# Kernel optimization log

Measured on AMD Instinct MI355X. Metric: run time of the kernel, lower is better.

## Reference

```python
import jax, jax.numpy as jnp
import numpy as np

N = 2048          # nodes == tokens
D_IN = 768        # input_size
H = 768           # hidden_size
OUT = 128         # output_size
NUM_LEVELS = int(np.floor(np.log2(N))) + 1  # heap tree height + 1 = 12


def _build_tree():
    # binary-heap tree: parent of node i (i>0) is (i-1)//2; node 0 is root
    parent = np.array([(i - 1) // 2 for i in range(1, N)], dtype=np.int64)
    child = np.arange(1, N, dtype=np.int64)
    # node_order = subtree height (leaves = 0), computed bottom-up
    node_order = np.zeros(N, dtype=np.int64)
    for i in range(N - 1, 0, -1):
        p = (i - 1) // 2
        node_order[p] = max(node_order[p], node_order[i] + 1)
    adjacency_list = np.stack([parent, child], axis=1)  # [E,2] (parent, child)
    edge_order = node_order[parent]                     # level of the parent
    return node_order, adjacency_list, edge_order


def setup_inputs() -> dict:
    key = jax.random.key(0)
    ks = jax.random.split(key, 16)
    s_in = 1.0 / np.sqrt(D_IN)
    s_h = 1.0 / np.sqrt(H)
    node_order, adjacency_list, edge_order = _build_tree()
    return {
        "tree_features": jax.random.normal(ks[0], (N, D_IN), jnp.float32),
        "features_tensor": jax.random.normal(ks[1], (N, D_IN), jnp.float32),
        # TreeLSTM params (child-sum)
        "W_iou": jax.random.normal(ks[2], (3 * H, D_IN), jnp.float32) * s_in,
        "b_iou": jax.random.normal(ks[3], (3 * H,), jnp.float32) * s_in,
        "U_iou": jax.random.normal(ks[4], (3 * H, H), jnp.float32) * s_h,
        "W_f": jax.random.normal(ks[5], (H, D_IN), jnp.float32) * s_in,
        "b_f": jax.random.normal(ks[6], (H,), jnp.float32) * s_in,
        "U_f": jax.random.normal(ks[7], (H, H), jnp.float32) * s_h,
        # nn.LSTM params (single layer, gate order i,f,g,o)
        "W_ih": jax.random.normal(ks[8], (4 * H, D_IN), jnp.float32) * s_h,
        "b_ih": jax.random.normal(ks[9], (4 * H,), jnp.float32) * s_h,
        "W_hh": jax.random.normal(ks[10], (4 * H, H), jnp.float32) * s_h,
        "b_hh": jax.random.normal(ks[11], (4 * H,), jnp.float32) * s_h,
        # classifier
        "W_cls": jax.random.normal(ks[12], (OUT, 2 * H), jnp.float32) * (1.0 / np.sqrt(2 * H)),
        "b_cls": jax.random.normal(ks[13], (OUT,), jnp.float32) * (1.0 / np.sqrt(2 * H)),
        "node_order": jnp.asarray(node_order),
        "adjacency_list": jnp.asarray(adjacency_list),
        "edge_order": jnp.asarray(edge_order),
    }


def _tree_lstm(x, node_order, adjacency_list, edge_order, W_iou, b_iou, U_iou, W_f, b_f, U_f):
    n, h_dim = x.shape[0], U_f.shape[0]
    x_iou = x @ W_iou.T + b_iou   # [N,3H]
    x_f = x @ W_f.T + b_f         # [N,H]
    parent = adjacency_list[:, 0]
    child = adjacency_list[:, 1]
    h = jnp.zeros((n, h_dim), x.dtype)
    c = jnp.zeros((n, h_dim), x.dtype)
    for lvl in range(NUM_LEVELS):
        emask = (edge_order == lvl).astype(x.dtype)[:, None]   # [E,1]
        child_h = h[child]
        child_c = c[child]
        h_sum = jax.ops.segment_sum(child_h * emask, parent, num_segments=n)
        iou = x_iou + h_sum @ U_iou.T
        i, o, u = jnp.split(iou, 3, axis=1)
        i = jax.nn.sigmoid(i); o = jax.nn.sigmoid(o); u = jnp.tanh(u)
        f = jax.nn.sigmoid(x_f[parent] + child_h @ U_f.T)       # per-edge forget gate
        c_sum = jax.ops.segment_sum(f * child_c * emask, parent, num_segments=n)
        c_new = i * u + c_sum
        h_new = o * jnp.tanh(c_new)
        nmask = (node_order == lvl)[:, None]
        h = jnp.where(nmask, h_new, h)
        c = jnp.where(nmask, c_new, c)
    return h, c


def _seq_lstm(x, W_ih, b_ih, W_hh, b_hh):
    h_dim = W_hh.shape[1]
    def step(carry, x_t):
        h_t, c_t = carry
        g = W_ih @ x_t + b_ih + W_hh @ h_t + b_hh
        i, f, gg, o = jnp.split(g, 4)
        i = jax.nn.sigmoid(i); f = jax.nn.sigmoid(f)
        gg = jnp.tanh(gg); o = jax.nn.sigmoid(o)
        c_t = f * c_t + i * gg
        h_t = o * jnp.tanh(c_t)
        return (h_t, c_t), h_t
    init = (jnp.zeros((h_dim,), x.dtype), jnp.zeros((h_dim,), x.dtype))
    _, hs = jax.lax.scan(step, init, x)
    return hs  # [N,H]


def reference(tree_features, features_tensor, W_iou, b_iou, U_iou, W_f, b_f, U_f,
              W_ih, b_ih, W_hh, b_hh, W_cls, b_cls,
              node_order, adjacency_list, edge_order):
    tree_h, _ = _tree_lstm(tree_features, node_order, adjacency_list, edge_order,
                           W_iou, b_iou, U_iou, W_f, b_f, U_f)
    lstm_h = _seq_lstm(features_tensor, W_ih, b_ih, W_hh, b_hh)
    cls_in = jnp.concatenate([tree_h, lstm_h], axis=1)          # [N,2H]
    logits = cls_in @ W_cls.T + b_cls                           # [N,OUT]
    return jax.nn.log_softmax(logits, axis=0)                   # LogSoftmax over dim=0
```

## Files before the change

### kernel.cpp

```cpp
#include <hip/hip_runtime.h>
#include <stdint.h>


typedef __bf16 bf16x8 __attribute__((ext_vector_type(8)));
typedef float  f32x4  __attribute__((ext_vector_type(4)));
typedef unsigned long long u64;

__device__ __forceinline__ float bf2f(uint16_t v) {
    return __uint_as_float(((uint32_t)v) << 16);
}
__device__ __forceinline__ uint16_t f2bf(float f) {
    uint32_t u = __float_as_uint(f);
    uint32_t r = (u + 0x7fffu + ((u >> 16) & 1u)) >> 16;
    return (uint16_t)r;
}
__device__ __forceinline__ float sigf(float x) { return 1.0f / (1.0f + __expf(-x)); }
__device__ __forceinline__ float tanh_f(float x) {
    x = fminf(fmaxf(x, -15.0f), 15.0f);
    float e = __expf(2.0f * x);
    return (e - 1.0f) / (e + 1.0f);
}

__global__ __launch_bounds__(256)
void detect_mode(const uint16_t* __restrict__ p, int* __restrict__ mode)
{
    int i = blockIdx.x * 256 + threadIdx.x;
    uint16_t v = p[i];
    bool bad = ((v >> 7) & 0xFF) == 0xFF;
    if (__ballot(bad) != 0ull) {
        if ((threadIdx.x & 63) == 0) atomicOr(mode, 1);
    }
}

struct ConvArgs {
    const void* src[14];
    void*       dst[14];
    int         n[14];
};

__global__ __launch_bounds__(256)
void conv_canon(ConvArgs a, const int* __restrict__ mode)
{
    int t = blockIdx.y;
    int n = a.n[t];
    int i = (blockIdx.x * 256 + threadIdx.x) * 8;
    if (i >= n) return;
    uint16_t* d = (uint16_t*)a.dst[t] + i;
    if (*mode) {
        const float* s = (const float*)a.src[t] + i;
        float4 v0 = reinterpret_cast<const float4*>(s)[0];
        float4 v1 = reinterpret_cast<const float4*>(s)[1];
        d[0] = f2bf(v0.x); d[1] = f2bf(v0.y); d[2] = f2bf(v0.z); d[3] = f2bf(v0.w);
        d[4] = f2bf(v1.x); d[5] = f2bf(v1.y); d[6] = f2bf(v1.z); d[7] = f2bf(v1.w);
    } else {
        *reinterpret_cast<uint4*>(d) =
            *reinterpret_cast<const uint4*>((const uint16_t*)a.src[t] + i);
    }
}

__global__ __launch_bounds__(256)
void gemm_pre(const uint16_t* __restrict__ treeF, const uint16_t* __restrict__ featF,
              const uint16_t* __restrict__ W_iou, const uint16_t* __restrict__ b_iou,
              const uint16_t* __restrict__ W_f,   const uint16_t* __restrict__ b_f,
              const uint16_t* __restrict__ W_ih,  const uint16_t* __restrict__ b_ih,
              const uint16_t* __restrict__ b_hh,
              uint16_t* __restrict__ x_iou, uint16_t* __restrict__ x_f,
              uint16_t* __restrict__ seq_pre)
{
    int lane = threadIdx.x & 63;
    int wave = threadIdx.x >> 6;
    int colTile = blockIdx.x * 4 + wave;
    int row0 = blockIdx.y * 16;
    int cl = lane & 15, quad = lane >> 4;
    int colg = colTile * 16;

    const uint16_t* A; const uint16_t* W; int wrow;
    if (colTile < 144)      { A = treeF; W = W_iou; wrow = colg; }
    else if (colTile < 192) { A = treeF; W = W_f;   wrow = colg - 2304; }
    else                    { A = featF; W = W_ih;  wrow = colg - 3072; }

    const uint16_t* arow = A + (size_t)(row0 + cl) * 768 + quad * 8;
    const uint16_t* brow = W + (size_t)(wrow + cl) * 768 + quad * 8;

    f32x4 acc = {0.f, 0.f, 0.f, 0.f};
    for (int k = 0; k < 768; k += 32) {
        bf16x8 a = *reinterpret_cast<const bf16x8*>(arow + k);
        bf16x8 b = *reinterpret_cast<const bf16x8*>(brow + k);
        acc = __builtin_amdgcn_mfma_f32_16x16x32_bf16(a, b, acc, 0, 0, 0);
    }

    int outcol = colg + cl;
    float bias; uint16_t* dst; int ldc; int ccol;
    if (colTile < 144)      { bias = bf2f(b_iou[outcol]); dst = x_iou; ldc = 2304; ccol = outcol; }
    else if (colTile < 192) { int c = outcol - 2304; bias = bf2f(b_f[c]); dst = x_f; ldc = 768;  ccol = c; }
    else {
        int c = outcol - 3072;
        int g = c / 768, j = c - g * 768;
        bias = bf2f(b_ih[c]) + bf2f(b_hh[c]);
        dst = seq_pre; ldc = 3072;
        ccol = (j >> 5) * 128 + g * 32 + (j & 31);
    }
    for (int r = 0; r < 4; ++r) {
        int row = row0 + quad * 4 + r;
        dst[(size_t)row * ldc + ccol] = f2bf(acc[r] + bias);
    }
}

__global__ __launch_bounds__(256)
void tree_dots_mfma(int s, int m,
                    const uint16_t* __restrict__ U_iou, const uint16_t* __restrict__ U_f,
                    const uint16_t* __restrict__ x_f,
                    uint16_t* __restrict__ x_iou, uint16_t* __restrict__ fdot,
                    const uint16_t* __restrict__ hb)
{
    int lane = threadIdx.x & 63;
    int wave = threadIdx.x >> 6;
    int cl = lane & 15, quad = lane >> 4;
    int mt1 = (m + 15) >> 4;
    int mt2 = (2 * m + 15) >> 4;
    int t1 = mt1 * 144;
    int tile = blockIdx.x * 4 + wave;
    if (tile >= t1 + mt2 * 48) return;

    if (tile < t1) {
        int rt = tile / 144, ct = tile - rt * 144;
        int pl = rt * 16 + cl; if (pl > m - 1) pl = m - 1;
        int p = s + pl;
        const uint16_t* a1 = hb + (size_t)(2 * p + 1) * 768 + quad * 8;
        const uint16_t* a2 = hb + (size_t)(2 * p + 2) * 768 + quad * 8;
        const uint16_t* brow = U_iou + (size_t)(ct * 16 + cl) * 768 + quad * 8;
        f32x4 acc = {0.f, 0.f, 0.f, 0.f};
        for (int k = 0; k < 768; k += 32) {
            bf16x8 b = *reinterpret_cast<const bf16x8*>(brow + k);
            acc = __builtin_amdgcn_mfma_f32_16x16x32_bf16(
                      *reinterpret_cast<const bf16x8*>(a1 + k), b, acc, 0, 0, 0);
            acc = __builtin_amdgcn_mfma_f32_16x16x32_bf16(
                      *reinterpret_cast<const bf16x8*>(a2 + k), b, acc, 0, 0, 0);
        }
        int outcol = ct * 16 + cl;
        #pragma unroll
        for (int r = 0; r < 4; ++r) {
            int prow = rt * 16 + quad * 4 + r;
            if (prow < m) {
                size_t off = (size_t)(s + prow) * 2304 + outcol;
                x_iou[off] = f2bf(bf2f(x_iou[off]) + acc[r]);
            }
        }
    } else {
        int t2i = tile - t1;
        int rt = t2i / 48, ct = t2i - rt * 48;
        int c0 = 2 * s + 1;
        int rl = rt * 16 + cl; if (rl > 2 * m - 1) rl = 2 * m - 1;
        const uint16_t* a = hb + (size_t)(c0 + rl) * 768 + quad * 8;
        const uint16_t* brow = U_f + (size_t)(ct * 16 + cl) * 768 + quad * 8;
        f32x4 acc = {0.f, 0.f, 0.f, 0.f};
        for (int k = 0; k < 768; k += 32) {
            acc = __builtin_amdgcn_mfma_f32_16x16x32_bf16(
                      *reinterpret_cast<const bf16x8*>(a + k),
                      *reinterpret_cast<const bf16x8*>(brow + k), acc, 0, 0, 0);
        }
        int outcol = ct * 16 + cl;
        #pragma unroll
        for (int r = 0; r < 4; ++r) {
            int rr = rt * 16 + quad * 4 + r;
            int c = c0 + rr;
            if (rr < 2 * m && c < 2048) {
                int p = (c - 1) >> 1;
                fdot[(size_t)c * 768 + outcol] =
                    f2bf(bf2f(x_f[(size_t)p * 768 + outcol]) + acc[r]);
            }
        }
    }
}

__global__ __launch_bounds__(256)
void tree_combine(int s, int m, const uint16_t* __restrict__ x_iou,
                  const uint16_t* __restrict__ fdot,
                  uint16_t* __restrict__ tree_hb, float* __restrict__ tree_c)
{
    int id = blockIdx.x * 256 + threadIdx.x;
    int pl = id / 768;
    int j = id - pl * 768;
    int p = s + pl;
    const uint16_t* iou = x_iou + (size_t)p * 2304;
    float iv = sigf(bf2f(iou[j]));
    float ov = sigf(bf2f(iou[768 + j]));
    float uv = tanh_f(bf2f(iou[1536 + j]));
    float csum = 0.f;
    int c1 = 2 * p + 1, c2 = 2 * p + 2;
    if (c1 < 2048) csum += sigf(bf2f(fdot[(size_t)c1 * 768 + j])) * tree_c[(size_t)c1 * 768 + j];
    if (c2 < 2048) csum += sigf(bf2f(fdot[(size_t)c2 * 768 + j])) * tree_c[(size_t)c2 * 768 + j];
    float c = iv * uv + csum;
    tree_c[(size_t)p * 768 + j] = c;
    tree_hb[(size_t)p * 768 + j] = f2bf(ov * tanh_f(c));
}

#define SEQ_WGS 24
#define SEQ_LAUNCH 256
__global__ __launch_bounds__(1024)
void seq_lstm(const uint16_t* __restrict__ W_hh, const uint16_t* __restrict__ seq_pre,
              uint16_t* __restrict__ hsb, u64* __restrict__ h_comm, int* __restrict__ ctl)
{
    __shared__ uint16_t hb16[2][768];
    __shared__ float    part[2][128];
    __shared__ int      s_slot;

    int tid = threadIdx.x;

    int xcc;
    asm("s_getreg_b32 %0, hwreg(HW_REG_XCC_ID)" : "=s"(xcc));
    if (tid == 0) {
        int tgt = atomicCAS(&ctl[1], -1, xcc);
        if (tgt == -1) tgt = xcc;
        int slot;
        if (xcc == tgt) {
            slot = atomicAdd(&ctl[0], 1);
        } else {
            int it = 0;
            for (;;) {
                int tk = __hip_atomic_load(&ctl[0], __ATOMIC_RELAXED,
                                           __HIP_MEMORY_SCOPE_AGENT);
                if (tk >= SEQ_WGS) { slot = 0x7fffffff; break; }
                if (++it > 2000) { slot = atomicAdd(&ctl[0], 1); break; }
                __builtin_amdgcn_s_sleep(8);
            }
        }
        s_slot = slot;
    }
    __syncthreads();
    int bid = s_slot;
    if (bid >= SEQ_WGS) return;

    int lane = tid & 63;
    int w    = tid >> 6;
    int tile = w >> 1;
    int khalf = w & 1;
    int tg = tile >> 1;
    int tj = (tile & 1) * 16 + (lane & 15);
    int rglob = tg * 768 + bid * 32 + tj;

    bf16x8 wq[12];
    {
        const uint16_t* src = W_hh + (size_t)rglob * 768 + khalf * 384 + (lane >> 4) * 8;
        #pragma unroll
        for (int i = 0; i < 12; ++i)
            wq[i] = *reinterpret_cast<const bf16x8*>(src + i * 32);
    }

    float cstate = 0.f;

    for (int t = 0; t < 2048; ++t) {
        float p0 = 0.f, p1 = 0.f, p2 = 0.f, p3 = 0.f;
        if (tid < 32) {
            const uint16_t* sp = seq_pre + (size_t)t * 3072 + bid * 128 + tid;
            p0 = bf2f(sp[0]);  p1 = bf2f(sp[32]);
            p2 = bf2f(sp[64]); p3 = bf2f(sp[96]);
        }

        uint16_t* hb = hb16[t & 1];
        if (t > 0) {
            if (tid < 384) {
                const u64* hw = h_comm + (size_t)((t - 1) & 1) * 384 + tid;
                u64 a;
                int guard = 0;
                for (;;) {
                    a = __hip_atomic_load(hw, __ATOMIC_RELAXED,
                                          __HIP_MEMORY_SCOPE_AGENT);
                    if ((uint32_t)(a >> 32) >= (uint32_t)t) break;
                    if (++guard > (1 << 22)) break;
                    __builtin_amdgcn_s_sleep(1);
                }
                hb[2 * tid]     = (uint16_t)a;
                hb[2 * tid + 1] = (uint16_t)(a >> 16);
            }
        } else {
            if (tid < 768) hb[tid] = 0;
        }
        __syncthreads();

        {
            const uint16_t* hbase = hb + khalf * 384 + (lane >> 4) * 8;
            f32x4 acc = {0.f, 0.f, 0.f, 0.f};
            #pragma unroll
            for (int ks = 0; ks < 12; ++ks) {
                bf16x8 hf = *reinterpret_cast<const bf16x8*>(hbase + ks * 32);
                acc = __builtin_amdgcn_mfma_f32_16x16x32_bf16(hf, wq[ks], acc, 0, 0, 0);
            }
            if ((lane >> 4) == 0)
                part[khalf][tile * 16 + lane] = acc[0];
        }
        __syncthreads();

        if (tid < 32) {
            int jl = tid;
            float gi = part[0][jl]      + part[1][jl]      + p0;
            float gf = part[0][32 + jl] + part[1][32 + jl] + p1;
            float gg = part[0][64 + jl] + part[1][64 + jl] + p2;
            float go = part[0][96 + jl] + part[1][96 + jl] + p3;

            float iv = sigf(gi), fv = sigf(gf), gv = tanh_f(gg), ov = sigf(go);
            cstate = fv * cstate + iv * gv;
            float hv = ov * tanh_f(cstate);

            uint32_t hb16v = (uint32_t)f2bf(hv);
            uint32_t hv_hi = __shfl(hb16v, 2 * (tid >> 1) + 1);
            uint32_t hv_lo = __shfl(hb16v, 2 * (tid >> 1));
            if ((tid & 1) == 0) {
                int q = tid >> 1;
                int wdx = bid * 16 + q;
                u64 wd = ((u64)(uint32_t)(t + 1) << 32)
                       | ((u64)hv_hi << 16) | (u64)hv_lo;
                __hip_atomic_store(h_comm + (size_t)(t & 1) * 384 + wdx, wd,
                                   __ATOMIC_RELAXED, __HIP_MEMORY_SCOPE_AGENT);
            }
            int j = bid * 32 + jl;
            hsb[(size_t)t * 768 + j] = (uint16_t)hb16v;
        }
    }
}

__global__ __launch_bounds__(256)
void cls_mfma(const uint16_t* __restrict__ hbT, const uint16_t* __restrict__ hsb,
              const uint16_t* __restrict__ W_cls, const uint16_t* __restrict__ b_cls,
              float* __restrict__ logits)
{
    int lane = threadIdx.x & 63;
    int wave = threadIdx.x >> 6;
    int cl = lane & 15, quad = lane >> 4;
    int tile = blockIdx.x * 4 + wave;
    int rt = tile >> 3, ct = tile & 7;
    const uint16_t* a1 = hbT + (size_t)(rt * 16 + cl) * 768 + quad * 8;
    const uint16_t* a2 = hsb + (size_t)(rt * 16 + cl) * 768 + quad * 8;
    const uint16_t* brow = W_cls + (size_t)(ct * 16 + cl) * 1536 + quad * 8;
    f32x4 acc = {0.f, 0.f, 0.f, 0.f};
    for (int k = 0; k < 768; k += 32) {
        acc = __builtin_amdgcn_mfma_f32_16x16x32_bf16(
                  *reinterpret_cast<const bf16x8*>(a1 + k),
                  *reinterpret_cast<const bf16x8*>(brow + k), acc, 0, 0, 0);
        acc = __builtin_amdgcn_mfma_f32_16x16x32_bf16(
                  *reinterpret_cast<const bf16x8*>(a2 + k),
                  *reinterpret_cast<const bf16x8*>(brow + 768 + k), acc, 0, 0, 0);
    }
    int outcol = ct * 16 + cl;
    float bias = bf2f(b_cls[outcol]);
    #pragma unroll
    for (int r = 0; r < 4; ++r) {
        int n = rt * 16 + quad * 4 + r;
        logits[(size_t)n * 128 + outcol] = acc[r] + bias;
    }
}

__global__ __launch_bounds__(256)
void col_softmax(const float* __restrict__ logits, void* __restrict__ out,
                 const int* __restrict__ mode)
{
    __shared__ float sred[256];
    int o = blockIdx.x, tid = threadIdx.x;
    float v[8];
    float mx = -1e30f;
    #pragma unroll
    for (int i = 0; i < 8; ++i) {
        v[i] = logits[(size_t)(i * 256 + tid) * 128 + o];
        mx = fmaxf(mx, v[i]);
    }
    sred[tid] = mx; __syncthreads();
    for (int s2 = 128; s2 > 0; s2 >>= 1) {
        if (tid < s2) sred[tid] = fmaxf(sred[tid], sred[tid + s2]);
        __syncthreads();
    }
    float M = sred[0]; __syncthreads();
    float sm = 0.f;
    #pragma unroll
    for (int i = 0; i < 8; ++i) sm += __expf(v[i] - M);
    sred[tid] = sm; __syncthreads();
    for (int s2 = 128; s2 > 0; s2 >>= 1) {
        if (tid < s2) sred[tid] += sred[tid + s2];
        __syncthreads();
    }
    float lse = M + logf(sred[0]);
    bool fp32 = (*mode != 0);
    #pragma unroll
    for (int i = 0; i < 8; ++i) {
        size_t idx = (size_t)(i * 256 + tid) * 128 + o;
        float val = v[i] - lse;
        if (fp32) ((float*)out)[idx] = val;
        else      ((uint16_t*)out)[idx] = f2bf(val);
    }
}

extern "C" void kernel_launch(void* const* d_in, const int* in_sizes, int n_in,
                              void* d_out, int out_size, void* d_ws, size_t ws_size,
                              hipStream_t stream)
{
    char* ws = (char*)d_ws;

    static const int   CN[14] = {1572864, 1572864, 1769472, 1769472, 589824, 589824,
                                 2359296, 2359296, 196608, 2304, 768, 3072, 3072, 128};
    static const size_t COFF[14] = {0, 1572864, 3145728, 4915200, 6684672, 7274496,
                                    7864320, 10223616, 12582912, 12779520, 12781824,
                                    12782592, 12785664, 12788736};
    static const int SRCI[14] = {0, 1, 2, 4, 5, 7, 8, 10, 12, 3, 6, 9, 11, 13};

    uint16_t* canon = (uint16_t*)ws;
    const uint16_t* treeF = canon + COFF[0];
    const uint16_t* featF = canon + COFF[1];
    const uint16_t* W_iou = canon + COFF[2];
    const uint16_t* U_iou = canon + COFF[3];
    const uint16_t* W_f   = canon + COFF[4];
    const uint16_t* U_f   = canon + COFF[5];
    const uint16_t* W_ih  = canon + COFF[6];
    const uint16_t* W_hh  = canon + COFF[7];
    const uint16_t* W_cls = canon + COFF[8];
    const uint16_t* b_iou = canon + COFF[9];
    const uint16_t* b_f   = canon + COFF[10];
    const uint16_t* b_ih  = canon + COFF[11];
    const uint16_t* b_hh  = canon + COFF[12];
    const uint16_t* b_cls = canon + COFF[13];

    const size_t CANON_B = 25577728;
    uint16_t* x_iou   = (uint16_t*)(ws + CANON_B);
    uint16_t* seq_pre = (uint16_t*)(ws + CANON_B + 9437184);
    uint16_t* x_f     = (uint16_t*)(ws + CANON_B + 22020096);
    uint16_t* fdot    = (uint16_t*)(ws + CANON_B + 25165824);
    uint16_t* tree_hb = (uint16_t*)(ws + CANON_B + 28311552);
    float*    tree_c  = (float*)   (ws + CANON_B + 31458816);
    uint16_t* hs_b    = (uint16_t*)(ws + CANON_B + 37750272);
    float*    logits  = (float*)   (ws + CANON_B + 40896000);
    u64*      h_comm  = (u64*)     (ws + CANON_B + 41944576);
    int*      mode    = (int*)     (ws + CANON_B + 41956864);
    int*      ctl     = mode + 16;
    const size_t WS_NEEDED = CANON_B + 41957120;
    if (ws_size < WS_NEEDED) return;

    hipMemsetAsync(h_comm, 0, 12288 + 256, stream);
    hipMemsetAsync(ctl + 1, 0xFF, 4, stream);
    hipMemsetAsync(tree_hb + (size_t)2048 * 768, 0, 1536, stream);

    detect_mode<<<256, 256, 0, stream>>>((const uint16_t*)d_in[0], mode);

    ConvArgs ca;
    for (int i = 0; i < 14; ++i) {
        ca.src[i] = d_in[SRCI[i]];
        ca.dst[i] = canon + COFF[i];
        ca.n[i]   = CN[i];
    }
    conv_canon<<<dim3(1152, 14), 256, 0, stream>>>(ca, mode);

    gemm_pre<<<dim3(96, 128), 256, 0, stream>>>(treeF, featF, W_iou, b_iou, W_f, b_f,
                                                W_ih, b_ih, b_hh, x_iou, x_f, seq_pre);

    tree_combine<<<1024 * 3, 256, 0, stream>>>(1024, 1024, x_iou, fdot, tree_hb, tree_c);
    for (int lvl = 1; lvl <= 11; ++lvl) {
        int s = (lvl == 11) ? 0 : (1 << (10 - lvl));
        int m = (lvl == 11) ? 1 : (1 << (10 - lvl));
        int mt1 = (m + 15) >> 4, mt2 = (2 * m + 15) >> 4;
        int tiles = mt1 * 144 + mt2 * 48;
        tree_dots_mfma<<<(tiles + 3) / 4, 256, 0, stream>>>(s, m, U_iou, U_f, x_f,
                                                            x_iou, fdot, tree_hb);
        tree_combine<<<m * 3, 256, 0, stream>>>(s, m, x_iou, fdot, tree_hb, tree_c);
    }

    seq_lstm<<<SEQ_LAUNCH, 1024, 0, stream>>>(W_hh, seq_pre, hs_b, h_comm, ctl);

    cls_mfma<<<256, 256, 0, stream>>>(tree_hb, hs_b, W_cls, b_cls, logits);
    col_softmax<<<128, 256, 0, stream>>>(logits, d_out, mode);
}
```

Baseline: 3.574 ms.

## Restructure sequential LSTM so each wave computes full-K gates and cell update locally

The recurrent LSTM kernel now uses 8 waves instead of 16. Each wave holds the full 768-wide K slice of W_hh for 4 hidden units across all four gates, so it no longer splits K across two waves and no longer reduces partial sums through shared memory. Gate values are exchanged within the wave by shuffles and every wave runs its own cell update and publishes h. This removes one __syncthreads and an LDS round trip from each of the 2048 serial steps, at the cost of twice the weight registers per thread and four MFMA accumulator chains.

```diff
diff --git a/kernel.cpp b/kernel.cpp
--- a/kernel.cpp
+++ b/kernel.cpp
@@ -197,12 +197,11 @@
 
 #define SEQ_WGS 24
 #define SEQ_LAUNCH 256
-__global__ __launch_bounds__(1024)
+__global__ __launch_bounds__(512)
 void seq_lstm(const uint16_t* __restrict__ W_hh, const uint16_t* __restrict__ seq_pre,
               uint16_t* __restrict__ hsb, u64* __restrict__ h_comm, int* __restrict__ ctl)
 {
     __shared__ uint16_t hb16[2][768];
-    __shared__ float    part[2][128];
     __shared__ int      s_slot;
 
     int tid = threadIdx.x;
@@ -232,32 +231,29 @@
     if (bid >= SEQ_WGS) return;
 
     int lane = tid & 63;
-    int w    = tid >> 6;
-    int tile = w >> 1;
-    int khalf = w & 1;
-    int tg = tile >> 1;
-    int tj = (tile & 1) * 16 + (lane & 15);
-    int rglob = tg * 768 + bid * 32 + tj;
-
-    bf16x8 wq[12];
+    int wv   = tid >> 6;
+    int cl   = lane & 15;
+    int quad = lane >> 4;
+    int g    = cl >> 2;
+    int jj   = lane & 3;
+    int j0   = bid * 32 + wv * 4;
+    int rglob = g * 768 + j0 + (cl & 3);
+    int preOff = bid * 128 + g * 32 + (wv * 4 + (cl & 3));
+
+    bf16x8 wq[24];
     {
-        const uint16_t* src = W_hh + (size_t)rglob * 768 + khalf * 384 + (lane >> 4) * 8;
+        const uint16_t* src = W_hh + (size_t)rglob * 768 + quad * 8;
         #pragma unroll
-        for (int i = 0; i < 12; ++i)
+        for (int i = 0; i < 24; ++i)
             wq[i] = *reinterpret_cast<const bf16x8*>(src + i * 32);
     }
 
     float cstate = 0.f;
 
     for (int t = 0; t < 2048; ++t) {
-        float p0 = 0.f, p1 = 0.f, p2 = 0.f, p3 = 0.f;
-        if (tid < 32) {
-            const uint16_t* sp = seq_pre + (size_t)t * 3072 + bid * 128 + tid;
-            p0 = bf2f(sp[0]);  p1 = bf2f(sp[32]);
-            p2 = bf2f(sp[64]); p3 = bf2f(sp[96]);
-        }
-
+        float pre = bf2f(seq_pre[(size_t)t * 3072 + preOff]);
         uint16_t* hb = hb16[t & 1];
+
         if (t > 0) {
             if (tid < 384) {
                 const u64* hw = h_comm + (size_t)((t - 1) & 1) * 384 + tid;
@@ -274,48 +270,46 @@
                 hb[2 * tid + 1] = (uint16_t)(a >> 16);
             }
         } else {
-            if (tid < 768) hb[tid] = 0;
+            if (tid < 384) { hb[2 * tid] = 0; hb[2 * tid + 1] = 0; }
         }
         __syncthreads();
 
-        {
-            const uint16_t* hbase = hb + khalf * 384 + (lane >> 4) * 8;
-            f32x4 acc = {0.f, 0.f, 0.f, 0.f};
-            #pragma unroll
-            for (int ks = 0; ks < 12; ++ks) {
-                bf16x8 hf = *reinterpret_cast<const bf16x8*>(hbase + ks * 32);
-                acc = __builtin_amdgcn_mfma_f32_16x16x32_bf16(hf, wq[ks], acc, 0, 0, 0);
-            }
-            if ((lane >> 4) == 0)
-                part[khalf][tile * 16 + lane] = acc[0];
-        }
-        __syncthreads();
-
-        if (tid < 32) {
-            int jl = tid;
-            float gi = part[0][jl]      + part[1][jl]      + p0;
-            float gf = part[0][32 + jl] + part[1][32 + jl] + p1;
-            float gg = part[0][64 + jl] + part[1][64 + jl] + p2;
-            float go = part[0][96 + jl] + part[1][96 + jl] + p3;
-
-            float iv = sigf(gi), fv = sigf(gf), gv = tanh_f(gg), ov = sigf(go);
-            cstate = fv * cstate + iv * gv;
-            float hv = ov * tanh_f(cstate);
-
-            uint32_t hb16v = (uint32_t)f2bf(hv);
-            uint32_t hv_hi = __shfl(hb16v, 2 * (tid >> 1) + 1);
-            uint32_t hv_lo = __shfl(hb16v, 2 * (tid >> 1));
-            if ((tid & 1) == 0) {
-                int q = tid >> 1;
-                int wdx = bid * 16 + q;
-                u64 wd = ((u64)(uint32_t)(t + 1) << 32)
-                       | ((u64)hv_hi << 16) | (u64)hv_lo;
-                __hip_atomic_store(h_comm + (size_t)(t & 1) * 384 + wdx, wd,
-                                   __ATOMIC_RELAXED, __HIP_MEMORY_SCOPE_AGENT);
-            }
-            int j = bid * 32 + jl;
-            hsb[(size_t)t * 768 + j] = (uint16_t)hb16v;
-        }
+        const uint16_t* hbase = hb + quad * 8;
+        f32x4 a0 = {0.f,0.f,0.f,0.f}, a1 = {0.f,0.f,0.f,0.f};
+        f32x4 a2 = {0.f,0.f,0.f,0.f}, a3 = {0.f,0.f,0.f,0.f};
+        #pragma unroll
+        for (int ks = 0; ks < 24; ks += 4) {
+            a0 = __builtin_amdgcn_mfma_f32_16x16x32_bf16(
+                     *reinterpret_cast<const bf16x8*>(hbase + (ks + 0) * 32), wq[ks + 0], a0, 0, 0, 0);
+            a1 = __builtin_amdgcn_mfma_f32_16x16x32_bf16(
+                     *reinterpret_cast<const bf16x8*>(hbase + (ks + 1) * 32), wq[ks + 1], a1, 0, 0, 0);
+            a2 = __builtin_amdgcn_mfma_f32_16x16x32_bf16(
+                     *reinterpret_cast<const bf16x8*>(hbase + (ks + 2) * 32), wq[ks + 2], a2, 0, 0, 0);
+            a3 = __builtin_amdgcn_mfma_f32_16x16x32_bf16(
+                     *reinterpret_cast<const bf16x8*>(hbase + (ks + 3) * 32), wq[ks + 3], a3, 0, 0, 0);
+        }
+        float gate = (a0[0] + a1[0]) + (a2[0] + a3[0]) + pre;
+
+        float gi = __shfl(gate, jj);
+        float gf = __shfl(gate, 4 + jj);
+        float gg = __shfl(gate, 8 + jj);
+        float go = __shfl(gate, 12 + jj);
+
+        float iv = sigf(gi), fv = sigf(gf), gv = tanh_f(gg), ov = sigf(go);
+        cstate = fv * cstate + iv * gv;
+        float hv = ov * tanh_f(cstate);
+
+        uint32_t hvb  = (uint32_t)f2bf(hv);
+        uint32_t hvhi = __shfl(hvb, jj | 1);
+        if (lane == 0 || lane == 2) {
+            int wdx = bid * 16 + wv * 2 + (jj >> 1);
+            u64 wd = ((u64)(uint32_t)(t + 1) << 32)
+                   | ((u64)hvhi << 16) | (u64)hvb;
+            __hip_atomic_store(h_comm + (size_t)(t & 1) * 384 + wdx, wd,
+                               __ATOMIC_RELAXED, __HIP_MEMORY_SCOPE_AGENT);
+        }
+        if (lane < 4)
+            hsb[(size_t)t * 768 + j0 + jj] = (uint16_t)hvb;
     }
 }
 
@@ -460,7 +454,7 @@
         tree_combine<<<m * 3, 256, 0, stream>>>(s, m, x_iou, fdot, tree_hb, tree_c);
     }
 
-    seq_lstm<<<SEQ_LAUNCH, 1024, 0, stream>>>(W_hh, seq_pre, hs_b, h_comm, ctl);
+    seq_lstm<<<SEQ_LAUNCH, 512, 0, stream>>>(W_hh, seq_pre, hs_b, h_comm, ctl);
 
     cls_mfma<<<256, 256, 0, stream>>>(tree_hb, hs_b, W_cls, b_cls, logits);
     col_softmax<<<128, 256, 0, stream>>>(logits, d_out, mode);
```

Result: slower. 4.645 ms (+30.0%).

## Run tree LSTM levels on idle helper workgroups inside the sequential LSTM kernel

Applied to the files above, without the earlier changes.

Merges the per-level tree_dots and tree_combine launches into the persistent seq_lstm kernel, renamed mega. The workgroups that are not among the 24 sequential-LSTM workers become helpers. They process the tree levels in a grid-strided way and synchronise with software barriers built on atomic counters. The aim is to overlap the tree LSTM with the latency-bound sequential recurrence and to remove about two dozen small kernel launches. The cost is that the software barriers need all helper groups resident at once, and the helpers' memory traffic may contend with the sequential critical path. An unused dot8 helper is also added.

```diff
diff --git a/kernel.cpp b/kernel.cpp
--- a/kernel.cpp
+++ b/kernel.cpp
@@ -19,6 +19,17 @@
     x = fminf(fmaxf(x, -15.0f), 15.0f);
     float e = __expf(2.0f * x);
     return (e - 1.0f) / (e + 1.0f);
+}
+__device__ __forceinline__ float dot8(uint4 w, const float* h, float acc) {
+    acc = fmaf(__uint_as_float(w.x << 16),          h[0], acc);
+    acc = fmaf(__uint_as_float(w.x & 0xffff0000u),  h[1], acc);
+    acc = fmaf(__uint_as_float(w.y << 16),          h[2], acc);
+    acc = fmaf(__uint_as_float(w.y & 0xffff0000u),  h[3], acc);
+    acc = fmaf(__uint_as_float(w.z << 16),          h[4], acc);
+    acc = fmaf(__uint_as_float(w.z & 0xffff0000u),  h[5], acc);
+    acc = fmaf(__uint_as_float(w.w << 16),          h[6], acc);
+    acc = fmaf(__uint_as_float(w.w & 0xffff0000u),  h[7], acc);
+    return acc;
 }
 
 __global__ __launch_bounds__(256)
@@ -106,21 +117,14 @@
     }
 }
 
-__global__ __launch_bounds__(256)
-void tree_dots_mfma(int s, int m,
-                    const uint16_t* __restrict__ U_iou, const uint16_t* __restrict__ U_f,
-                    const uint16_t* __restrict__ x_f,
-                    uint16_t* __restrict__ x_iou, uint16_t* __restrict__ fdot,
-                    const uint16_t* __restrict__ hb)
-{
-    int lane = threadIdx.x & 63;
-    int wave = threadIdx.x >> 6;
+__device__ __forceinline__ void dots_tile(int tile, int s, int m, int lane,
+        const uint16_t* __restrict__ U_iou, const uint16_t* __restrict__ U_f,
+        const uint16_t* __restrict__ x_f, uint16_t* __restrict__ x_iou,
+        uint16_t* __restrict__ fdot, const uint16_t* __restrict__ hb)
+{
     int cl = lane & 15, quad = lane >> 4;
     int mt1 = (m + 15) >> 4;
-    int mt2 = (2 * m + 15) >> 4;
     int t1 = mt1 * 144;
-    int tile = blockIdx.x * 4 + wave;
-    if (tile >= t1 + mt2 * 48) return;
 
     if (tile < t1) {
         int rt = tile / 144, ct = tile - rt * 144;
@@ -173,15 +177,10 @@
     }
 }
 
-__global__ __launch_bounds__(256)
-void tree_combine(int s, int m, const uint16_t* __restrict__ x_iou,
-                  const uint16_t* __restrict__ fdot,
-                  uint16_t* __restrict__ tree_hb, float* __restrict__ tree_c)
-{
-    int id = blockIdx.x * 256 + threadIdx.x;
-    int pl = id / 768;
-    int j = id - pl * 768;
-    int p = s + pl;
+__device__ __forceinline__ void combine_elem(int p, int j,
+        const uint16_t* __restrict__ x_iou, const uint16_t* __restrict__ fdot,
+        uint16_t* __restrict__ tree_hb, float* __restrict__ tree_c)
+{
     const uint16_t* iou = x_iou + (size_t)p * 2304;
     float iv = sigf(bf2f(iou[j]));
     float ov = sigf(bf2f(iou[768 + j]));
@@ -197,13 +196,19 @@
 
 #define SEQ_WGS 24
 #define SEQ_LAUNCH 256
+#define NHELP (SEQ_LAUNCH - SEQ_WGS)
+
 __global__ __launch_bounds__(1024)
-void seq_lstm(const uint16_t* __restrict__ W_hh, const uint16_t* __restrict__ seq_pre,
-              uint16_t* __restrict__ hsb, u64* __restrict__ h_comm, int* __restrict__ ctl)
+void mega(const uint16_t* __restrict__ W_hh, const uint16_t* __restrict__ seq_pre,
+          uint16_t* __restrict__ hsb, u64* __restrict__ h_comm, int* __restrict__ ctl,
+          const uint16_t* __restrict__ U_iou, const uint16_t* __restrict__ U_f,
+          const uint16_t* __restrict__ x_f, uint16_t* __restrict__ x_iou,
+          uint16_t* __restrict__ fdot, uint16_t* __restrict__ tree_hb,
+          float* __restrict__ tree_c, int* __restrict__ tcnt)
 {
     __shared__ uint16_t hb16[2][768];
     __shared__ float    part[2][128];
-    __shared__ int      s_slot;
+    __shared__ int      s_slot, s_hid;
 
     int tid = threadIdx.x;
 
@@ -226,95 +231,149 @@
             }
         }
         s_slot = slot;
+        if (slot >= SEQ_WGS) s_hid = atomicAdd(&ctl[3], 1);
     }
     __syncthreads();
     int bid = s_slot;
-    if (bid >= SEQ_WGS) return;
-
-    int lane = tid & 63;
-    int w    = tid >> 6;
-    int tile = w >> 1;
-    int khalf = w & 1;
-    int tg = tile >> 1;
-    int tj = (tile & 1) * 16 + (lane & 15);
-    int rglob = tg * 768 + bid * 32 + tj;
-
-    bf16x8 wq[12];
-    {
-        const uint16_t* src = W_hh + (size_t)rglob * 768 + khalf * 384 + (lane >> 4) * 8;
-        #pragma unroll
-        for (int i = 0; i < 12; ++i)
-            wq[i] = *reinterpret_cast<const bf16x8*>(src + i * 32);
-    }
-
-    float cstate = 0.f;
-
-    for (int t = 0; t < 2048; ++t) {
-        float p0 = 0.f, p1 = 0.f, p2 = 0.f, p3 = 0.f;
-        if (tid < 32) {
-            const uint16_t* sp = seq_pre + (size_t)t * 3072 + bid * 128 + tid;
-            p0 = bf2f(sp[0]);  p1 = bf2f(sp[32]);
-            p2 = bf2f(sp[64]); p3 = bf2f(sp[96]);
-        }
-
-        uint16_t* hb = hb16[t & 1];
-        if (t > 0) {
-            if (tid < 384) {
-                const u64* hw = h_comm + (size_t)((t - 1) & 1) * 384 + tid;
-                u64 a;
-                int guard = 0;
-                for (;;) {
-                    a = __hip_atomic_load(hw, __ATOMIC_RELAXED,
-                                          __HIP_MEMORY_SCOPE_AGENT);
-                    if ((uint32_t)(a >> 32) >= (uint32_t)t) break;
-                    if (++guard > (1 << 22)) break;
-                    __builtin_amdgcn_s_sleep(1);
+
+    if (bid < SEQ_WGS) {
+        int lane = tid & 63;
+        int w    = tid >> 6;
+        int tile = w >> 1;
+        int khalf = w & 1;
+        int tg = tile >> 1;
+        int tj = (tile & 1) * 16 + (lane & 15);
+        int rglob = tg * 768 + bid * 32 + tj;
+
+        bf16x8 wq[12];
+        {
+            const uint16_t* src = W_hh + (size_t)rglob * 768 + khalf * 384 + (lane >> 4) * 8;
+            #pragma unroll
+            for (int i = 0; i < 12; ++i)
+                wq[i] = *reinterpret_cast<const bf16x8*>(src + i * 32);
+        }
+
+        float cstate = 0.f;
+
+        for (int t = 0; t < 2048; ++t) {
+            float p0 = 0.f, p1 = 0.f, p2 = 0.f, p3 = 0.f;
+            if (tid < 32) {
+                const uint16_t* sp = seq_pre + (size_t)t * 3072 + bid * 128 + tid;
+                p0 = bf2f(sp[0]);  p1 = bf2f(sp[32]);
+                p2 = bf2f(sp[64]); p3 = bf2f(sp[96]);
+            }
+
+            uint16_t* hb = hb16[t & 1];
+            if (t > 0) {
+                if (tid < 384) {
+                    const u64* hw = h_comm + (size_t)((t - 1) & 1) * 384 + tid;
+                    u64 a;
+                    int guard = 0;
+                    for (;;) {
+                        a = __hip_atomic_load(hw, __ATOMIC_RELAXED,
+                                              __HIP_MEMORY_SCOPE_AGENT);
+                        if ((uint32_t)(a >> 32) >= (uint32_t)t) break;
+                        if (++guard > (1 << 22)) break;
+                        __builtin_amdgcn_s_sleep(1);
+                    }
+                    hb[2 * tid]     = (uint16_t)a;
+                    hb[2 * tid + 1] = (uint16_t)(a >> 16);
                 }
-                hb[2 * tid]     = (uint16_t)a;
-                hb[2 * tid + 1] = (uint16_t)(a >> 16);
-            }
-        } else {
-            if (tid < 768) hb[tid] = 0;
-        }
-        __syncthreads();
-
-        {
-            const uint16_t* hbase = hb + khalf * 384 + (lane >> 4) * 8;
-            f32x4 acc = {0.f, 0.f, 0.f, 0.f};
-            #pragma unroll
-            for (int ks = 0; ks < 12; ++ks) {
-                bf16x8 hf = *reinterpret_cast<const bf16x8*>(hbase + ks * 32);
-                acc = __builtin_amdgcn_mfma_f32_16x16x32_bf16(hf, wq[ks], acc, 0, 0, 0);
-            }
-            if ((lane >> 4) == 0)
-                part[khalf][tile * 16 + lane] = acc[0];
-        }
-        __syncthreads();
-
-        if (tid < 32) {
-            int jl = tid;
-            float gi = part[0][jl]      + part[1][jl]      + p0;
-            float gf = part[0][32 + jl] + part[1][32 + jl] + p1;
-            float gg = part[0][64 + jl] + part[1][64 + jl] + p2;
-            float go = part[0][96 + jl] + part[1][96 + jl] + p3;
-
-            float iv = sigf(gi), fv = sigf(gf), gv = tanh_f(gg), ov = sigf(go);
-            cstate = fv * cstate + iv * gv;
-            float hv = ov * tanh_f(cstate);
-
-            uint32_t hb16v = (uint32_t)f2bf(hv);
-            uint32_t hv_hi = __shfl(hb16v, 2 * (tid >> 1) + 1);
-            uint32_t hv_lo = __shfl(hb16v, 2 * (tid >> 1));
-            if ((tid & 1) == 0) {
-                int q = tid >> 1;
-                int wdx = bid * 16 + q;
-                u64 wd = ((u64)(uint32_t)(t + 1) << 32)
-                       | ((u64)hv_hi << 16) | (u64)hv_lo;
-                __hip_atomic_store(h_comm + (size_t)(t & 1) * 384 + wdx, wd,
-                                   __ATOMIC_RELAXED, __HIP_MEMORY_SCOPE_AGENT);
-            }
-            int j = bid * 32 + jl;
-            hsb[(size_t)t * 768 + j] = (uint16_t)hb16v;
+            } else {
+                if (tid < 768) hb[tid] = 0;
+            }
+            __syncthreads();
+
+            {
+                const uint16_t* hbase = hb + khalf * 384 + (lane >> 4) * 8;
+                f32x4 acc = {0.f, 0.f, 0.f, 0.f};
+                #pragma unroll
+                for (int ks = 0; ks < 12; ++ks) {
+                    bf16x8 hf = *reinterpret_cast<const bf16x8*>(hbase + ks * 32);
+                    acc = __builtin_amdgcn_mfma_f32_16x16x32_bf16(hf, wq[ks], acc, 0, 0, 0);
+                }
+                if ((lane >> 4) == 0)
+                    part[khalf][tile * 16 + lane] = acc[0];
+            }
+            __syncthreads();
+
+            if (tid < 32) {
+                int jl = tid;
+                float gi = part[0][jl]      + part[1][jl]      + p0;
+                float gf = part[0][32 + jl] + part[1][32 + jl] + p1;
+                float gg = part[0][64 + jl] + part[1][64 + jl] + p2;
+                float go = part[0][96 + jl] + part[1][96 + jl] + p3;
+
+                float iv = sigf(gi), fv = sigf(gf), gv = tanh_f(gg), ov = sigf(go);
+                cstate = fv * cstate + iv * gv;
+                float hv = ov * tanh_f(cstate);
+
+                uint32_t hb16v = (uint32_t)f2bf(hv);
+                uint32_t hv_hi = __shfl(hb16v, 2 * (tid >> 1) + 1);
+                uint32_t hv_lo = __shfl(hb16v, 2 * (tid >> 1));
+                if ((tid & 1) == 0) {
+                    int q = tid >> 1;
+                    int wdx = bid * 16 + q;
+                    u64 wd = ((u64)(uint32_t)(t + 1) << 32)
+                           | ((u64)hv_hi << 16) | (u64)hv_lo;
+                    __hip_atomic_store(h_comm + (size_t)(t & 1) * 384 + wdx, wd,
+                                       __ATOMIC_RELAXED, __HIP_MEMORY_SCOPE_AGENT);
+                }
+                int j = bid * 32 + jl;
+                hsb[(size_t)t * 768 + j] = (uint16_t)hb16v;
+            }
+        }
+    } else {
+        int hid = s_hid;
+        int lane = tid & 63;
+        int wv = tid >> 6;
+
+        for (int i = hid * 1024 + tid; i < 1024 * 768; i += NHELP * 1024) {
+            combine_elem(1024 + i / 768, i - (i / 768) * 768, x_iou, fdot, tree_hb, tree_c);
+        }
+        for (int L = 1; L <= 11; ++L) {
+            {
+                int k = L - 1;
+                __threadfence();
+                __syncthreads();
+                if (tid == 0) {
+                    __hip_atomic_fetch_add(&tcnt[2 * k], 1, __ATOMIC_ACQ_REL,
+                                           __HIP_MEMORY_SCOPE_AGENT);
+                    int g2 = 0;
+                    while (__hip_atomic_load(&tcnt[2 * k], __ATOMIC_ACQUIRE,
+                                             __HIP_MEMORY_SCOPE_AGENT) < NHELP) {
+                        if (++g2 > (1 << 20)) break;
+                        __builtin_amdgcn_s_sleep(4);
+                    }
+                }
+                __syncthreads();
+                __threadfence();
+            }
+            int s = (L == 11) ? 0 : (1 << (10 - L));
+            int m = (L == 11) ? 1 : (1 << (10 - L));
+            int mt1 = (m + 15) >> 4, mt2 = (2 * m + 15) >> 4;
+            int ntiles = mt1 * 144 + mt2 * 48;
+            for (int tile = hid * 16 + wv; tile < ntiles; tile += NHELP * 16)
+                dots_tile(tile, s, m, lane, U_iou, U_f, x_f, x_iou, fdot, tree_hb);
+            {
+                int k = L - 1;
+                __threadfence();
+                __syncthreads();
+                if (tid == 0) {
+                    __hip_atomic_fetch_add(&tcnt[2 * k + 1], 1, __ATOMIC_ACQ_REL,
+                                           __HIP_MEMORY_SCOPE_AGENT);
+                    int g2 = 0;
+                    while (__hip_atomic_load(&tcnt[2 * k + 1], __ATOMIC_ACQUIRE,
+                                             __HIP_MEMORY_SCOPE_AGENT) < NHELP) {
+                        if (++g2 > (1 << 20)) break;
+                        __builtin_amdgcn_s_sleep(4);
+                    }
+                }
+                __syncthreads();
+                __threadfence();
+            }
+            for (int i = hid * 1024 + tid; i < m * 768; i += NHELP * 1024)
+                combine_elem(s + i / 768, i - (i / 768) * 768, x_iou, fdot, tree_hb, tree_c);
         }
     }
 }
@@ -429,12 +488,13 @@
     u64*      h_comm  = (u64*)     (ws + CANON_B + 41944576);
     int*      mode    = (int*)     (ws + CANON_B + 41956864);
     int*      ctl     = mode + 16;
+    int*      tcnt    = mode + 24;
     const size_t WS_NEEDED = CANON_B + 41957120;
     if (ws_size < WS_NEEDED) return;
 
-    hipMemsetAsync(h_comm, 0, 12288 + 256, stream);
-    hipMemsetAsync(ctl + 1, 0xFF, 4, stream);
-    hipMemsetAsync(tree_hb + (size_t)2048 * 768, 0, 1536, stream);
+    (void)hipMemsetAsync(h_comm, 0, 12288 + 256, stream);
+    (void)hipMemsetAsync(ctl + 1, 0xFF, 4, stream);
+    (void)hipMemsetAsync(tree_hb + (size_t)2048 * 768, 0, 1536, stream);
 
     detect_mode<<<256, 256, 0, stream>>>((const uint16_t*)d_in[0], mode);
 
@@ -449,18 +509,9 @@
     gemm_pre<<<dim3(96, 128), 256, 0, stream>>>(treeF, featF, W_iou, b_iou, W_f, b_f,
                                                 W_ih, b_ih, b_hh, x_iou, x_f, seq_pre);
 
-    tree_combine<<<1024 * 3, 256, 0, stream>>>(1024, 1024, x_iou, fdot, tree_hb, tree_c);
-    for (int lvl = 1; lvl <= 11; ++lvl) {
-        int s = (lvl == 11) ? 0 : (1 << (10 - lvl));
-        int m = (lvl == 11) ? 1 : (1 << (10 - lvl));
-        int mt1 = (m + 15) >> 4, mt2 = (2 * m + 15) >> 4;
-        int tiles = mt1 * 144 + mt2 * 48;
-        tree_dots_mfma<<<(tiles + 3) / 4, 256, 0, stream>>>(s, m, U_iou, U_f, x_f,
-                                                            x_iou, fdot, tree_hb);
-        tree_combine<<<m * 3, 256, 0, stream>>>(s, m, x_iou, fdot, tree_hb, tree_c);
-    }
-
-    seq_lstm<<<SEQ_LAUNCH, 1024, 0, stream>>>(W_hh, seq_pre, hs_b, h_comm, ctl);
+    mega<<<SEQ_LAUNCH, 1024, 0, stream>>>(W_hh, seq_pre, hs_b, h_comm, ctl,
+                                          U_iou, U_f, x_f, x_iou, fdot,
+                                          tree_hb, tree_c, tcnt);
 
     cls_mfma<<<256, 256, 0, stream>>>(tree_hb, hs_b, W_cls, b_cls, logits);
     col_softmax<<<128, 256, 0, stream>>>(logits, d_out, mode);
```

After: 4.838 ms. 1.35x slower.
